# Kernel optimization log

Measured on AMD Instinct MI355X. Metric: run time of the kernel, lower is better.

Reference implementation:

```python
import jax, jax.numpy as jnp
import numpy as np

ALPHA, GAMMA = 0.25, 2.0
COST_CLASS, COST_BBOX, COST_GIOU = 2.0, 5.0, 2.0
EPS = 1e-8


def box_cxcywh_to_xyxy(b):
    cx, cy, w, h = b[..., 0], b[..., 1], b[..., 2], b[..., 3]
    return jnp.stack([cx - 0.5 * w, cy - 0.5 * h, cx + 0.5 * w, cy + 0.5 * h], axis=-1)


def generalized_box_iou(boxes1, boxes2):
    # boxes1: [N,4] xyxy, boxes2: [M,4] xyxy -> [N,M] GIoU
    area1 = (boxes1[:, 2] - boxes1[:, 0]) * (boxes1[:, 3] - boxes1[:, 1])
    area2 = (boxes2[:, 2] - boxes2[:, 0]) * (boxes2[:, 3] - boxes2[:, 1])
    lt = jnp.maximum(boxes1[:, None, :2], boxes2[None, :, :2])   # [N,M,2]
    rb = jnp.minimum(boxes1[:, None, 2:], boxes2[None, :, 2:])   # [N,M,2]
    wh = jnp.clip(rb - lt, 0.0)
    inter = wh[..., 0] * wh[..., 1]
    union = area1[:, None] + area2[None, :] - inter
    iou = inter / union
    # smallest enclosing box
    lt_c = jnp.minimum(boxes1[:, None, :2], boxes2[None, :, :2])
    rb_c = jnp.maximum(boxes1[:, None, 2:], boxes2[None, :, 2:])
    wh_c = jnp.clip(rb_c - lt_c, 0.0)
    area_c = wh_c[..., 0] * wh_c[..., 1]
    return iou - (area_c - union) / area_c


def setup_inputs() -> dict:
    key = jax.random.key(0)
    k1, k2, k3, k4 = jax.random.split(key, 4)
    BS, NQ, NC, NT = 16, 900, 91, 960
    pred_logits = jax.random.normal(k1, (BS, NQ, NC), dtype=jnp.float32)
    pred_boxes = jax.random.uniform(k2, (BS, NQ, 4), dtype=jnp.float32)
    tgt_ids = jax.random.randint(k3, (NT,), 0, NC, dtype=jnp.int64)
    tgt_bbox = jax.random.uniform(k4, (NT, 4), dtype=jnp.float32)
    return {"pred_logits": pred_logits, "pred_boxes": pred_boxes,
            "tgt_ids": tgt_ids, "tgt_bbox": tgt_bbox}


def reference(pred_logits, pred_boxes, tgt_ids, tgt_bbox):
    bs, nq, _ = pred_logits.shape
    out_prob = jax.nn.sigmoid(pred_logits.reshape(bs * nq, -1))      # [BN, C]
    out_bbox = pred_boxes.reshape(bs * nq, 4)                         # [BN, 4]
    # focal-style classification cost, gathered at target class ids
    neg_cost = (1.0 - ALPHA) * out_prob ** GAMMA * (-jnp.log(1.0 - out_prob + EPS))
    pos_cost = ALPHA * (1.0 - out_prob) ** GAMMA * (-jnp.log(out_prob + EPS))
    cost_class = pos_cost[:, tgt_ids] - neg_cost[:, tgt_ids]          # [BN, NT]
    # pairwise L1 distance between boxes (cxcywh space), like torch.cdist(p=1)
    cost_bbox = jnp.sum(jnp.abs(out_bbox[:, None, :] - tgt_bbox[None, :, :]), axis=-1)
    cost_giou = -generalized_box_iou(box_cxcywh_to_xyxy(out_bbox),
                                     box_cxcywh_to_xyxy(tgt_bbox))    # [BN, NT]
    C = COST_BBOX * cost_bbox + COST_CLASS * cost_class + COST_GIOU * cost_giou
    return C.reshape(bs, nq, -1)
```

## Files before the change

kernel.cpp:

```cpp
#include <hip/hip_runtime.h>
#include <math.h>


#define ALPHA_F   0.25f
#define COST_CLS  2.0f
#define COST_BBOX 5.0f
#define COST_GIOU 2.0f
#define EPS_F     1e-8f

constexpr int THREADS = 256;

typedef float vfloat4 __attribute__((ext_vector_type(4)));

__device__ __forceinline__ float focal_entry(float x) {
    const float p  = 1.0f / (1.0f + __expf(-x));
    const float om = 1.0f - p;
    const float neg = (1.0f - ALPHA_F) * p * p * (-__logf(om + EPS_F));
    const float pos = ALPHA_F * om * om        * (-__logf(p  + EPS_F));
    return COST_CLS * (pos - neg) + COST_GIOU;
}

template<int NC, int NT>
__global__ __launch_bounds__(THREADS) void matcher_kernel_s(
    const float* __restrict__ logits,
    const float* __restrict__ boxes,
    const int*   __restrict__ tids,
    const float* __restrict__ tboxes,
    float*       __restrict__ out)
{
    constexpr int JPT = 4;
    constexpr int NJT = NT / JPT;

    __shared__ float s_cls[NC];

    const int tid = threadIdx.x;
    const int row = blockIdx.x;

    const int jb = (tid < NJT) ? tid : (NJT - 1);
    const int tt = (tid < NC)  ? tid : (NC - 1);

    const float x = logits[(size_t)row * NC + tt];
    const int4 tv = reinterpret_cast<const int4*>(tids)[jb];
    float4 tb[JPT];
    #pragma unroll
    for (int k = 0; k < JPT; ++k)
        tb[k] = reinterpret_cast<const float4*>(tboxes)[jb * JPT + k];
    const float4 pb = reinterpret_cast<const float4*>(boxes)[row];

    const float px0 = pb.x - 0.5f * pb.z, py0 = pb.y - 0.5f * pb.w;
    const float px1 = pb.x + 0.5f * pb.z, py1 = pb.y + 0.5f * pb.w;
    const float parea = pb.z * pb.w;

    float rv[JPT];
    #pragma unroll
    for (int k = 0; k < JPT; ++k) {
        const float4 t = tb[k];
        const float hw = 0.5f * t.z, hh = 0.5f * t.w;
        const float tx0 = t.x - hw, tx1 = t.x + hw;
        const float ty0 = t.y - hh, ty1 = t.y + hh;
        const float tarea = t.z * t.w;
        const float l1 = (fabsf(pb.x - t.x) + fabsf(pb.y - t.y))
                       + (fabsf(pb.z - t.z) + fabsf(pb.w - t.w));
        const float iwr = fminf(px1, tx1) - fmaxf(px0, tx0);
        const float ihr = fminf(py1, ty1) - fmaxf(py0, ty0);
        const float inter = fmaxf(iwr, 0.0f) * fmaxf(ihr, 0.0f);
        const float uni = (parea + tarea) - inter;
        const float cw = (pb.z + t.z) - iwr;
        const float ch = (pb.w + t.w) - ihr;
        const float carea = cw * ch;
        const float num  = fmaf(inter, carea, uni * uni);
        const float rcpd = __builtin_amdgcn_rcpf(uni * carea);
        rv[k] = fmaf(-2.0f * num, rcpd, COST_BBOX * l1);
    }

    const float fe = focal_entry(x);
    if (tid < NC) s_cls[tt] = fe;
    __syncthreads();

    if (tid >= NJT) return;

    const int ic[JPT] = {tv.x, tv.y, tv.z, tv.w};
    vfloat4 v;
    v.x = rv[0] + s_cls[ic[0]];
    v.y = rv[1] + s_cls[ic[1]];
    v.z = rv[2] + s_cls[ic[2]];
    v.w = rv[3] + s_cls[ic[3]];
    float* __restrict__ optr = out + (size_t)row * NT + tid * JPT;
    __builtin_nontemporal_store(v, reinterpret_cast<vfloat4*>(optr));
}

constexpr int GROWS = 8;
__global__ __launch_bounds__(THREADS) void matcher_kernel_g(
    const float* __restrict__ logits, const float* __restrict__ boxes,
    const int* __restrict__ tids, const float* __restrict__ tboxes,
    float* __restrict__ out, int BN, int NC, int NT)
{
    extern __shared__ float s_cls_g[];
    const int tid  = threadIdx.x;
    const int row0 = blockIdx.x * GROWS;
    const int nrows = (BN - row0 < GROWS) ? (BN - row0) : GROWS;

    for (int t = tid; t < nrows * NC; t += THREADS) {
        const int r = t / NC, c = t - r * NC;
        const float x = logits[(size_t)(row0 + r) * NC + c];
        const float p  = 1.0f / (1.0f + expf(-x));
        const float om = 1.0f - p;
        const float neg = (1.0f - ALPHA_F) * p * p * (-logf(om + EPS_F));
        const float pos = ALPHA_F * om * om        * (-logf(p + EPS_F));
        s_cls_g[r * NC + c] = pos - neg;
    }
    __syncthreads();

    for (int r = 0; r < nrows; ++r) {
        const int row = row0 + r;
        const float4 pb = reinterpret_cast<const float4*>(boxes)[row];
        const float px0 = pb.x - 0.5f * pb.z, py0 = pb.y - 0.5f * pb.w;
        const float px1 = pb.x + 0.5f * pb.z, py1 = pb.y + 0.5f * pb.w;
        const float parea = pb.z * pb.w;
        for (int j = tid; j < NT; j += THREADS) {
            const float4 b = reinterpret_cast<const float4*>(tboxes)[j];
            const float bx0 = b.x - 0.5f * b.z, by0 = b.y - 0.5f * b.w;
            const float bx1 = b.x + 0.5f * b.z, by1 = b.y + 0.5f * b.w;
            const float l1 = fabsf(pb.x - b.x) + fabsf(pb.y - b.y)
                           + fabsf(pb.z - b.z) + fabsf(pb.w - b.w);
            const float iw = fmaxf(fminf(px1, bx1) - fmaxf(px0, bx0), 0.0f);
            const float ih = fmaxf(fminf(py1, by1) - fmaxf(py0, by0), 0.0f);
            const float inter = iw * ih;
            const float uni = parea + b.z * b.w - inter;
            const float iou = inter / uni;
            const float cw = fmaxf(px1, bx1) - fminf(px0, bx0);
            const float ch = fmaxf(py1, by1) - fminf(py0, by0);
            const float carea = cw * ch;
            const float giou = iou - (carea - uni) / carea;
            const float ccls = s_cls_g[r * NC + tids[j]];
            out[(size_t)row * NT + j] = COST_BBOX * l1 + COST_CLS * ccls - COST_GIOU * giou;
        }
        __syncthreads();
    }
}

extern "C" void kernel_launch(void* const* d_in, const int* in_sizes, int n_in,
                              void* d_out, int out_size, void* d_ws, size_t ws_size,
                              hipStream_t stream) {
    const float* logits = (const float*)d_in[0];
    const float* boxes  = (const float*)d_in[1];
    const int*   tids   = (const int*)d_in[2];
    const float* tboxes = (const float*)d_in[3];
    float* out = (float*)d_out;

    const int BN = in_sizes[1] / 4;
    const int NC = in_sizes[0] / BN;
    const int NT = in_sizes[2];

    if (NC == 91 && NT == 960) {
        matcher_kernel_s<91, 960><<<BN, THREADS, 0, stream>>>(
            logits, boxes, tids, tboxes, out);
    } else {
        const int grid = (BN + GROWS - 1) / GROWS;
        const size_t shmem = (size_t)GROWS * NC * sizeof(float);
        matcher_kernel_g<<<grid, THREADS, shmem, stream>>>(
            logits, boxes, tids, tboxes, out, BN, NC, NT);
    }
}
```

Baseline: 23.94 us.

## Map one wavefront per row and drop block-wide barrier in matcher kernel

Restructures the specialized kernel so each 64-lane wave handles one output row, with four rows per block, instead of one row per 256-thread block. Each wave computes its own focal class table in a private shared-memory slice and uses only an LDS wait rather than __syncthreads, then loops over 15 targets per lane with coalesced scalar nontemporal stores. The intent is to remove idle threads (256 threads for 240 outputs before), drop block barriers, and cut the block count. In exchange it issues scalar rather than vector stores and reloads target boxes and ids per iteration, relying on the cache.

```diff
diff --git a/kernel.cpp b/kernel.cpp
--- a/kernel.cpp
+++ b/kernel.cpp
@@ -10,8 +10,6 @@
 
 constexpr int THREADS = 256;
 
-typedef float vfloat4 __attribute__((ext_vector_type(4)));
-
 __device__ __forceinline__ float focal_entry(float x) {
     const float p  = 1.0f / (1.0f + __expf(-x));
     const float om = 1.0f - p;
@@ -21,40 +19,49 @@
 }
 
 template<int NC, int NT>
-__global__ __launch_bounds__(THREADS) void matcher_kernel_s(
+__global__ __launch_bounds__(THREADS, 8) void matcher_kernel_w(
     const float* __restrict__ logits,
     const float* __restrict__ boxes,
     const int*   __restrict__ tids,
     const float* __restrict__ tboxes,
     float*       __restrict__ out)
 {
-    constexpr int JPT = 4;
-    constexpr int NJT = NT / JPT;
+    constexpr int NWAVE = THREADS / 64;
+    constexpr int JPT   = NT / 64;
+    constexpr int NCP   = 96;
 
-    __shared__ float s_cls[NC];
+    __shared__ float s_cls[NWAVE * NCP];
 
-    const int tid = threadIdx.x;
-    const int row = blockIdx.x;
+    const int tid  = threadIdx.x;
+    const int wave = tid >> 6;
+    const int lane = tid & 63;
+    const int row  = blockIdx.x * NWAVE + wave;
 
-    const int jb = (tid < NJT) ? tid : (NJT - 1);
-    const int tt = (tid < NC)  ? tid : (NC - 1);
+    float* const s_my = s_cls + wave * NCP;
 
-    const float x = logits[(size_t)row * NC + tt];
-    const int4 tv = reinterpret_cast<const int4*>(tids)[jb];
-    float4 tb[JPT];
-    #pragma unroll
-    for (int k = 0; k < JPT; ++k)
-        tb[k] = reinterpret_cast<const float4*>(tboxes)[jb * JPT + k];
+    const float* __restrict__ lg = logits + (size_t)row * NC;
+    const int i0 = (lane < NC) ? lane : (NC - 1);
+    const int i1 = (lane + 64 < NC) ? (lane + 64) : (NC - 1);
+    const float x0 = lg[i0];
+    const float x1 = lg[i1];
     const float4 pb = reinterpret_cast<const float4*>(boxes)[row];
+
+    const float f0 = focal_entry(x0);
+    const float f1 = focal_entry(x1);
+    if (lane < NC)      s_my[lane]      = f0;
+    if (lane + 64 < NC) s_my[lane + 64] = f1;
+    asm volatile("s_waitcnt lgkmcnt(0)" ::: "memory");
 
     const float px0 = pb.x - 0.5f * pb.z, py0 = pb.y - 0.5f * pb.w;
     const float px1 = pb.x + 0.5f * pb.z, py1 = pb.y + 0.5f * pb.w;
     const float parea = pb.z * pb.w;
 
-    float rv[JPT];
-    #pragma unroll
+    float* __restrict__ obase = out + (size_t)row * NT + lane;
+    #pragma unroll 3
     for (int k = 0; k < JPT; ++k) {
-        const float4 t = tb[k];
+        const int j = lane + k * 64;
+        const float4 t = reinterpret_cast<const float4*>(tboxes)[j];
+        const int   c  = tids[j];
         const float hw = 0.5f * t.z, hh = 0.5f * t.w;
         const float tx0 = t.x - hw, tx1 = t.x + hw;
         const float ty0 = t.y - hh, ty1 = t.y + hh;
@@ -70,23 +77,10 @@
         const float carea = cw * ch;
         const float num  = fmaf(inter, carea, uni * uni);
         const float rcpd = __builtin_amdgcn_rcpf(uni * carea);
-        rv[k] = fmaf(-2.0f * num, rcpd, COST_BBOX * l1);
+        const float base = fmaf(COST_BBOX, l1, s_my[c]);
+        const float v = fmaf(-2.0f * num, rcpd, base);
+        __builtin_nontemporal_store(v, obase + k * 64);
     }
-
-    const float fe = focal_entry(x);
-    if (tid < NC) s_cls[tt] = fe;
-    __syncthreads();
-
-    if (tid >= NJT) return;
-
-    const int ic[JPT] = {tv.x, tv.y, tv.z, tv.w};
-    vfloat4 v;
-    v.x = rv[0] + s_cls[ic[0]];
-    v.y = rv[1] + s_cls[ic[1]];
-    v.z = rv[2] + s_cls[ic[2]];
-    v.w = rv[3] + s_cls[ic[3]];
-    float* __restrict__ optr = out + (size_t)row * NT + tid * JPT;
-    __builtin_nontemporal_store(v, reinterpret_cast<vfloat4*>(optr));
 }
 
 constexpr int GROWS = 8;
@@ -152,8 +146,8 @@
     const int NC = in_sizes[0] / BN;
     const int NT = in_sizes[2];
 
-    if (NC == 91 && NT == 960) {
-        matcher_kernel_s<91, 960><<<BN, THREADS, 0, stream>>>(
+    if (NC == 91 && NT == 960 && BN % 4 == 0) {
+        matcher_kernel_w<91, 960><<<BN / 4, THREADS, 0, stream>>>(
             logits, boxes, tids, tboxes, out);
     } else {
         const int grid = (BN + GROWS - 1) / GROWS;
```

Measured after the change: 24.77 us. +3.5%, slower.
